# Kernel tuning notes

Hardware: AMD Instinct MI355X
Metric: run time of the kernel (lower is better)

The kernel has to match this reference:

```python
import jax, jax.numpy as jnp
import numpy as np

IN_DIM = 300   # GloVe embedding dim
MEM = 150      # TreeLSTM memory dim
K = 4          # children per internal node (complete K-ary tree)
D = 9          # number of levels (leaves = level 0, root = level D-1)
SIZES = [K ** (D - 1 - d) for d in range(D)]  # nodes per level, leaves first
N = sum(SIZES)  # 87381 total nodes


def setup_inputs() -> dict:
    key = jax.random.key(0)
    ks = jax.random.split(key, 18)
    s_in = 1.0 / np.sqrt(IN_DIM)
    s_m = 1.0 / np.sqrt(MEM)
    inp = {"embs": jax.random.normal(ks[0], (N, IN_DIM), jnp.float32)}
    i = 1
    for nm in ["ix", "fx", "ux", "ox"]:  # input->mem linears
        inp["W_" + nm] = jax.random.uniform(ks[i], (IN_DIM, MEM), jnp.float32, -s_in, s_in); i += 1
        inp["b_" + nm] = jax.random.uniform(ks[i], (MEM,), jnp.float32, -s_in, s_in); i += 1
    for nm in ["ih", "fh", "uh", "oh"]:  # mem->mem linears
        inp["W_" + nm] = jax.random.uniform(ks[i], (MEM, MEM), jnp.float32, -s_m, s_m); i += 1
        inp["b_" + nm] = jax.random.uniform(ks[i], (MEM,), jnp.float32, -s_m, s_m); i += 1
    return inp


def reference(embs, W_ix, b_ix, W_fx, b_fx, W_ux, b_ux, W_ox, b_ox,
              W_ih, b_ih, W_fh, b_fh, W_uh, b_uh, W_oh, b_oh):
    """Level-batched Child-Sum TreeLSTM over a complete K-ary forest.
    Nodes are stored leaves-first; children of parent p at level d are
    nodes p*K .. p*K+K-1 of level d-1. Returns h for all N nodes (root last)."""
    off = 0
    h_prev = c_prev = None
    h_all = []
    for d in range(D):
        n = SIZES[d]
        x = embs[off:off + n]                       # (n, IN_DIM)
        if d == 0:
            # leaves: zero child state -> child_h_sum = 0, f*child_c = 0
            h_sum = jnp.zeros((n, MEM), embs.dtype)
            fc = jnp.zeros((n, MEM), embs.dtype)
        else:
            ch = h_prev.reshape(n, K, MEM)          # child h, (n, K, MEM)
            cc = c_prev.reshape(n, K, MEM)          # child c
            h_sum = ch.sum(axis=1)                  # child-sum of h
            # per-child forget gate: fh(child_h) + fx(x)
            f = jax.nn.sigmoid(jnp.einsum('nkm,mp->nkp', ch, W_fh) + b_fh
                               + (x @ W_fx + b_fx)[:, None, :])
            fc = (f * cc).sum(axis=1)
        i_g = jax.nn.sigmoid(x @ W_ix + b_ix + h_sum @ W_ih + b_ih)
        o_g = jax.nn.sigmoid(x @ W_ox + b_ox + h_sum @ W_oh + b_oh)
        u = jnp.tanh(x @ W_ux + b_ux + h_sum @ W_uh + b_uh)
        c = i_g * u + fc
        h = o_g * jnp.tanh(c)
        h_all.append(h)
        h_prev, c_prev = h, c
        off += n
    return jnp.concatenate(h_all, axis=0)           # (N, MEM)
```

## Files before the change

kernel.cpp:

```cpp
#include <hip/hip_runtime.h>

#define MEM    150
#define GW     640
#define KX     300
#define KXP    320
#define KH     160
#define NLEAF  65536
#define NTOT   87381
#define DEPTH  9

static const int SIZES[DEPTH] = {65536,16384,4096,1024,256,64,16,4,1};
static const int OFF[DEPTH]   = {0,65536,81920,86016,87040,87296,87360,87376,87380};

typedef __attribute__((ext_vector_type(8))) short short8;
typedef __attribute__((ext_vector_type(4))) float f32x4;

__device__ __forceinline__ float sigf(float x) { return 1.0f / (1.0f + __expf(-x)); }
__device__ __forceinline__ float tanhf_fast(float x) {
    float e = __expf(2.0f * x);
    return 1.0f - 2.0f / (e + 1.0f);
}
__device__ __forceinline__ unsigned short f2bf(float f) {
    union { float f; unsigned u; } v; v.f = f;
    unsigned r = v.u + 0x7FFF + ((v.u >> 16) & 1);
    return (unsigned short)(r >> 16);
}
__device__ __forceinline__ float bf2f(unsigned short u) {
    union { unsigned u; float f; } v; v.u = ((unsigned)u) << 16; return v.f;
}

typedef const __attribute__((address_space(1))) unsigned int* as1_u32p;
typedef __attribute__((address_space(3))) unsigned int* as3_u32p;
__device__ __forceinline__ void gl_lds16(const unsigned short* g, unsigned short* l) {
    __builtin_amdgcn_global_load_lds((as1_u32p)g, (as3_u32p)l, 16, 0, 0);
}

__global__ void pack_weights(const float* __restrict__ Wix, const float* __restrict__ Wfx,
                             const float* __restrict__ Wux, const float* __restrict__ Wox,
                             const float* __restrict__ bix, const float* __restrict__ bfx,
                             const float* __restrict__ bux, const float* __restrict__ box,
                             const float* __restrict__ Wih, const float* __restrict__ Wfh,
                             const float* __restrict__ Wuh, const float* __restrict__ Woh,
                             const float* __restrict__ bfh,
                             unsigned short* __restrict__ W4xT, unsigned short* __restrict__ W4hT,
                             float* __restrict__ b4x, float* __restrict__ b4hf)
{
    int stride = gridDim.x * blockDim.x;
    int tid = blockIdx.x * blockDim.x + threadIdx.x;
    for (int idx = tid; idx < GW * KXP; idx += stride) {
        int c = idx / KXP, k = idx - c * KXP;
        int j = c >> 2, g = c & 3;
        const float* W = (g == 0) ? Wix : (g == 1) ? Wfx : (g == 2) ? Wux : Wox;
        W4xT[idx] = (j < MEM && k < KX) ? f2bf(W[k * MEM + j]) : (unsigned short)0;
    }
    for (int idx = tid; idx < GW * KH; idx += stride) {
        int c = idx / KH, k = idx - c * KH;
        int j = c >> 2, g = c & 3;
        const float* W = (g == 0) ? Wih : (g == 1) ? Wfh : (g == 2) ? Wuh : Woh;
        W4hT[idx] = (j < MEM && k < MEM) ? f2bf(W[k * MEM + j]) : (unsigned short)0;
    }
    for (int idx = tid; idx < GW; idx += stride) {
        int j = idx >> 2, g = idx & 3;
        const float* b = (g == 0) ? bix : (g == 1) ? bfx : (g == 2) ? bux : box;
        b4x[idx]  = (j < MEM) ? b[j] : 0.0f;
        b4hf[idx] = (g == 1 && j < MEM) ? bfh[j] : 0.0f;
    }
}

__global__ void conv_embs(const float* __restrict__ embs, unsigned short* __restrict__ Abf)
{
    int idx = blockIdx.x * 256 + threadIdx.x;
    if (idx >= NTOT * (KXP / 8)) return;
    int n = idx / (KXP / 8), c = idx - n * (KXP / 8);
    int c0 = c * 8;
    unsigned short v[8];
    if (c0 + 8 <= KX) {
        const float4* p = (const float4*)(embs + (size_t)n * KX + c0);
        float4 f0 = p[0], f1 = p[1];
        v[0]=f2bf(f0.x); v[1]=f2bf(f0.y); v[2]=f2bf(f0.z); v[3]=f2bf(f0.w);
        v[4]=f2bf(f1.x); v[5]=f2bf(f1.y); v[6]=f2bf(f1.z); v[7]=f2bf(f1.w);
    } else {
        const float* row = embs + (size_t)n * KX;
        #pragma unroll
        for (int j = 0; j < 8; ++j) {
            int col = c0 + j;
            v[j] = (col < KX) ? f2bf(row[col]) : (unsigned short)0;
        }
    }
    *(short8*)&Abf[(size_t)n * KXP + c0] = *(short8*)v;
}

__global__ __launch_bounds__(256) void gemm_xproj(
    const unsigned short* __restrict__ A,
    const unsigned short* __restrict__ BT,
    const float* __restrict__ bias,
    unsigned short* __restrict__ PG,
    const float* __restrict__ bih, const float* __restrict__ buh,
    const float* __restrict__ boh,
    float* __restrict__ outLeaf, float* __restrict__ CLeaf,
    unsigned short* __restrict__ HbfLeaf)
{
    __shared__ __align__(16) unsigned short lds[16384];
    unsigned short* As = lds;
    unsigned short* Bs = lds + 8192;

    const int nwg = gridDim.x;
    const int orig = blockIdx.x;
    const int qq = nwg >> 3, rr = nwg & 7;
    const int xcd = orig & 7, lin = orig >> 3;
    const int dd = (xcd < rr ? xcd * (qq + 1) : rr * (qq + 1) + (xcd - rr) * qq) + lin;
    const int mtile = dd / 5, ntile = dd - mtile * 5;

    const int t = threadIdx.x;
    const int m0 = mtile * 128, n0 = ntile * 128;
    const int l = t & 63, w = t >> 6;
    const int l15 = l & 15, q = l >> 4;
    const int wm = (w & 1) * 64, wn = (w >> 1) * 64;

    const int srow = t >> 2;
    const int scol = ((t & 3) ^ (srow & 3)) * 8;
    int gr0 = m0 + srow;      if (gr0 >= NTOT) gr0 = NTOT - 1;
    int gr1 = m0 + 64 + srow; if (gr1 >= NTOT) gr1 = NTOT - 1;
    const unsigned short* a0 = A + (size_t)gr0 * KXP + scol;
    const unsigned short* a1 = A + (size_t)gr1 * KXP + scol;
    const unsigned short* b0 = BT + (size_t)(n0 + srow) * KXP + scol;
    const unsigned short* b1 = BT + (size_t)(n0 + 64 + srow) * KXP + scol;

    f32x4 acc[4][4];
    #pragma unroll
    for (int i = 0; i < 4; ++i)
        #pragma unroll
        for (int j = 0; j < 4; ++j)
            acc[i][j] = (f32x4){0.f, 0.f, 0.f, 0.f};

    gl_lds16(a0, As + t * 8);
    gl_lds16(a1, As + 2048 + t * 8);
    gl_lds16(b0, Bs + t * 8);
    gl_lds16(b1, Bs + 2048 + t * 8);
    __syncthreads();

    int cur = 0;
    const int kiters = KXP >> 5;
    for (int kt = 0; kt < kiters; ++kt) {
        if (kt + 1 < kiters) {
            const int ko = (kt + 1) << 5;
            const int nb = cur ^ 1;
            gl_lds16(a0 + ko, As + nb * 4096 + t * 8);
            gl_lds16(a1 + ko, As + nb * 4096 + 2048 + t * 8);
            gl_lds16(b0 + ko, Bs + nb * 4096 + t * 8);
            gl_lds16(b1 + ko, Bs + nb * 4096 + 2048 + t * 8);
        }
        short8 a[4], b[4];
        const int csw = (q ^ (l15 & 3)) * 8;
        #pragma unroll
        for (int i = 0; i < 4; ++i)
            a[i] = *(const short8*)&As[cur * 4096 + (wm + i * 16 + l15) * 32 + csw];
        #pragma unroll
        for (int j = 0; j < 4; ++j)
            b[j] = *(const short8*)&Bs[cur * 4096 + (wn + j * 16 + l15) * 32 + csw];
        #pragma unroll
        for (int i = 0; i < 4; ++i)
            #pragma unroll
            for (int j = 0; j < 4; ++j)
                acc[i][j] = __builtin_amdgcn_mfma_f32_16x16x32_bf16(a[i], b[j], acc[i][j], 0, 0, 0);
        __syncthreads();
        cur ^= 1;
    }

    float bj[4];
    #pragma unroll
    for (int j = 0; j < 4; ++j) bj[j] = bias[n0 + wn + j * 16 + l15];
    #pragma unroll
    for (int i = 0; i < 4; ++i)
        #pragma unroll
        for (int j = 0; j < 4; ++j)
            #pragma unroll
            for (int r = 0; r < 4; ++r)
                lds[(wm + i * 16 + q * 4 + r) * 128 + wn + j * 16 + l15] =
                    f2bf(acc[i][j][r] + bj[j]);
    __syncthreads();

    if (m0 < NLEAF) {
        #pragma unroll
        for (int s = 0; s < 16; ++s) {
            int idx = (s << 8) + t;
            int row = idx >> 5, jl = idx & 31;
            int grow = m0 + row;
            int j = ntile * 32 + jl;
            const unsigned short* g4 = &lds[row * 128 + jl * 4];
            if (j < MEM) {
                float gi = bf2f(g4[0]) + bih[j];
                float gu = bf2f(g4[2]) + buh[j];
                float go = bf2f(g4[3]) + boh[j];
                float iv = sigf(gi), uv = tanhf_fast(gu), ov = sigf(go);
                float c = iv * uv;
                float h = ov * tanhf_fast(c);
                outLeaf[(size_t)grow * MEM + j] = h;
                CLeaf[(size_t)grow * MEM + j] = c;
                HbfLeaf[(size_t)grow * KH + j] = f2bf(h);
            } else if (j < KH) {
                HbfLeaf[(size_t)grow * KH + j] = 0;
            }
        }
    } else {
        int row = t >> 1, half = t & 1;
        int grow = m0 + row;
        if (grow < NTOT) {
            const unsigned short* src = &lds[row * 128 + half * 64];
            unsigned short* dst = PG + (size_t)grow * GW + n0 + half * 64;
            #pragma unroll
            for (int c8 = 0; c8 < 8; ++c8)
                *(short8*)(dst + c8 * 8) = *(const short8*)(src + c8 * 8);
        }
    }
}

__global__ __launch_bounds__(256) void gemm_level(
    const unsigned short* __restrict__ Hprev, int nprev, int npar,
    const unsigned short* __restrict__ BT, const float* __restrict__ bias,
    const unsigned short* __restrict__ P,
    const float* __restrict__ Cprev,
    const float* __restrict__ bih, const float* __restrict__ buh,
    const float* __restrict__ boh,
    float* __restrict__ outRow, float* __restrict__ Crow,
    unsigned short* __restrict__ HbfRow)
{
    __shared__ __align__(16) unsigned short lds[16384];
    unsigned short* As = lds;
    unsigned short* Bs = lds + 8192;

    const int nwg = gridDim.x;
    const int orig = blockIdx.x;
    const int qq = nwg >> 3, rr = nwg & 7;
    const int xcd = orig & 7, lin = orig >> 3;
    const int dd = (xcd < rr ? xcd * (qq + 1) : rr * (qq + 1) + (xcd - rr) * qq) + lin;
    const int mtile = dd / 5, ntile = dd - mtile * 5;

    const int t = threadIdx.x;
    const int m0 = mtile * 128, n0 = ntile * 128;
    const int l = t & 63, w = t >> 6;
    const int l15 = l & 15, q = l >> 4;
    const int wm = (w & 1) * 64, wn = (w >> 1) * 64;

    const int srow = t >> 2;
    const int scol = ((t & 3) ^ (srow & 3)) * 8;
    int gr0 = m0 + srow;      if (gr0 >= nprev) gr0 = nprev - 1;
    int gr1 = m0 + 64 + srow; if (gr1 >= nprev) gr1 = nprev - 1;
    const unsigned short* a0 = Hprev + (size_t)gr0 * KH + scol;
    const unsigned short* a1 = Hprev + (size_t)gr1 * KH + scol;
    const unsigned short* b0 = BT + (size_t)(n0 + srow) * KH + scol;
    const unsigned short* b1 = BT + (size_t)(n0 + 64 + srow) * KH + scol;

    f32x4 acc[4][4];
    #pragma unroll
    for (int i = 0; i < 4; ++i)
        #pragma unroll
        for (int j = 0; j < 4; ++j)
            acc[i][j] = (f32x4){0.f, 0.f, 0.f, 0.f};

    gl_lds16(a0, As + t * 8);
    gl_lds16(a1, As + 2048 + t * 8);
    gl_lds16(b0, Bs + t * 8);
    gl_lds16(b1, Bs + 2048 + t * 8);
    __syncthreads();

    int cur = 0;
    const int kiters = KH >> 5;
    for (int kt = 0; kt < kiters; ++kt) {
        if (kt + 1 < kiters) {
            const int ko = (kt + 1) << 5;
            const int nb = cur ^ 1;
            gl_lds16(a0 + ko, As + nb * 4096 + t * 8);
            gl_lds16(a1 + ko, As + nb * 4096 + 2048 + t * 8);
            gl_lds16(b0 + ko, Bs + nb * 4096 + t * 8);
            gl_lds16(b1 + ko, Bs + nb * 4096 + 2048 + t * 8);
        }
        short8 a[4], b[4];
        const int csw = (q ^ (l15 & 3)) * 8;
        #pragma unroll
        for (int i = 0; i < 4; ++i)
            a[i] = *(const short8*)&As[cur * 4096 + (wm + i * 16 + l15) * 32 + csw];
        #pragma unroll
        for (int j = 0; j < 4; ++j)
            b[j] = *(const short8*)&Bs[cur * 4096 + (wn + j * 16 + l15) * 32 + csw];
        #pragma unroll
        for (int i = 0; i < 4; ++i)
            #pragma unroll
            for (int j = 0; j < 4; ++j)
                acc[i][j] = __builtin_amdgcn_mfma_f32_16x16x32_bf16(a[i], b[j], acc[i][j], 0, 0, 0);
        __syncthreads();
        cur ^= 1;
    }

    float bj[4];
    #pragma unroll
    for (int j = 0; j < 4; ++j) bj[j] = bias[n0 + wn + j * 16 + l15];
    #pragma unroll
    for (int i = 0; i < 4; ++i)
        #pragma unroll
        for (int j = 0; j < 4; ++j)
            #pragma unroll
            for (int r = 0; r < 4; ++r)
                lds[(wm + i * 16 + q * 4 + r) * 128 + wn + j * 16 + l15] =
                    f2bf(acc[i][j][r] + bj[j]);
    __syncthreads();

    const int pp0 = m0 >> 2;
    #pragma unroll
    for (int s = 0; s < 4; ++s) {
        int idx = (s << 8) + t;
        int pl = idx >> 5, jl = idx & 31;
        int par = pp0 + pl;
        if (par >= npar) continue;
        int j = ntile * 32 + jl;
        if (j < MEM) {
            const unsigned short* xr = P + (size_t)par * GW + 4 * j;
            float ip = bf2f(xr[0]) + bih[j];
            float fx = bf2f(xr[1]);
            float up = bf2f(xr[2]) + buh[j];
            float op = bf2f(xr[3]) + boh[j];
            float fc = 0.0f;
            #pragma unroll
            for (int k = 0; k < 4; ++k) {
                const unsigned short* g4 = &lds[(pl * 4 + k) * 128 + jl * 4];
                ip += bf2f(g4[0]);
                up += bf2f(g4[2]);
                op += bf2f(g4[3]);
                float f = sigf(fx + bf2f(g4[1]));
                fc += f * Cprev[(size_t)(4 * par + k) * MEM + j];
            }
            float iv = sigf(ip), uv = tanhf_fast(up), ov = sigf(op);
            float c = iv * uv + fc;
            float h = ov * tanhf_fast(c);
            outRow[(size_t)par * MEM + j] = h;
            Crow[(size_t)par * MEM + j] = c;
            HbfRow[(size_t)par * KH + j] = f2bf(h);
        } else if (j < KH) {
            HbfRow[(size_t)par * KH + j] = 0;
        }
    }
}

extern "C" void kernel_launch(void* const* d_in, const int* in_sizes, int n_in,
                              void* d_out, int out_size, void* d_ws, size_t ws_size,
                              hipStream_t stream)
{
    (void)in_sizes; (void)n_in; (void)out_size;
    const float* embs = (const float*)d_in[0];
    const float* Wix = (const float*)d_in[1];  const float* bix = (const float*)d_in[2];
    const float* Wfx = (const float*)d_in[3];  const float* bfx = (const float*)d_in[4];
    const float* Wux = (const float*)d_in[5];  const float* bux = (const float*)d_in[6];
    const float* Wox = (const float*)d_in[7];  const float* box = (const float*)d_in[8];
    const float* Wih = (const float*)d_in[9];  const float* bih = (const float*)d_in[10];
    const float* Wfh = (const float*)d_in[11]; const float* bfh = (const float*)d_in[12];
    const float* Wuh = (const float*)d_in[13]; const float* buh = (const float*)d_in[14];
    const float* Woh = (const float*)d_in[15]; const float* boh = (const float*)d_in[16];
    float* out = (float*)d_out;

    char* p = (char*)d_ws;
    auto alloc = [&](size_t bytes) -> char* {
        char* r = p;
        p += (bytes + 255) & ~(size_t)255;
        return r;
    };
    unsigned short* PG   = (unsigned short*)alloc((size_t)NTOT * GW * 2);
    float*          C    = (float*)alloc((size_t)NTOT * MEM * 4);
    unsigned short* Hbf  = (unsigned short*)alloc((size_t)NTOT * KH * 2);
    unsigned short* W4xT = (unsigned short*)alloc((size_t)GW * KXP * 2);
    unsigned short* W4hT = (unsigned short*)alloc((size_t)GW * KH * 2);
    float*          b4x  = (float*)alloc(GW * 4);
    float*          b4hf = (float*)alloc(GW * 4);
    if ((size_t)(p - (char*)d_ws) > ws_size) return;

    unsigned short* Abf = PG;

    pack_weights<<<128, 256, 0, stream>>>(Wix, Wfx, Wux, Wox, bix, bfx, bux, box,
                                          Wih, Wfh, Wuh, Woh, bfh,
                                          W4xT, W4hT, b4x, b4hf);

    conv_embs<<<(NTOT * (KXP / 8) + 255) / 256, 256, 0, stream>>>(embs, Abf);

    {
        int mt = (NTOT + 127) / 128;
        gemm_xproj<<<mt * 5, 256, 0, stream>>>(
            Abf, W4xT, b4x, PG, bih, buh, boh, out, C, Hbf);
    }

    for (int d = 1; d < DEPTH; ++d) {
        int nprev = SIZES[d - 1];
        int n = SIZES[d];
        int mt = (nprev + 127) / 128;
        gemm_level<<<mt * 5, 256, 0, stream>>>(
            Hbf + (size_t)OFF[d - 1] * KH, nprev, n,
            W4hT, b4hf,
            PG + (size_t)OFF[d] * GW,
            C + (size_t)OFF[d - 1] * MEM,
            bih, buh, boh,
            out + (size_t)OFF[d] * MEM, C + (size_t)OFF[d] * MEM,
            Hbf + (size_t)OFF[d] * KH);
    }
}
```

Before: 371.8 us.

## Merge weight packing and embedding conversion; use 512-thread GEMM blocks with 8 waves

Combines the weight-pack and embedding bf16 conversion kernels into one launch by splitting blocks by index. Both GEMM kernels move from 256 to 512 threads per block. Each of the 8 waves now computes a 64x32 sub-tile instead of 64x64, and each thread issues one A and one B LDS load per k-step instead of two. The aim is to cut per-wave register and accumulator pressure, add more waves to hide latency, and save one launch. The cost is lower MFMA reuse per wave and more waves contending at each block barrier.

Result: faster. 349.9 us (-5.9%).

```diff
diff --git a/kernel.cpp b/kernel.cpp
--- a/kernel.cpp
+++ b/kernel.cpp
@@ -35,62 +35,63 @@
     __builtin_amdgcn_global_load_lds((as1_u32p)g, (as3_u32p)l, 16, 0, 0);
 }
 
-__global__ void pack_weights(const float* __restrict__ Wix, const float* __restrict__ Wfx,
-                             const float* __restrict__ Wux, const float* __restrict__ Wox,
-                             const float* __restrict__ bix, const float* __restrict__ bfx,
-                             const float* __restrict__ bux, const float* __restrict__ box,
-                             const float* __restrict__ Wih, const float* __restrict__ Wfh,
-                             const float* __restrict__ Wuh, const float* __restrict__ Woh,
-                             const float* __restrict__ bfh,
-                             unsigned short* __restrict__ W4xT, unsigned short* __restrict__ W4hT,
-                             float* __restrict__ b4x, float* __restrict__ b4hf)
+__global__ void prep(const float* __restrict__ Wix, const float* __restrict__ Wfx,
+                     const float* __restrict__ Wux, const float* __restrict__ Wox,
+                     const float* __restrict__ bix, const float* __restrict__ bfx,
+                     const float* __restrict__ bux, const float* __restrict__ box,
+                     const float* __restrict__ Wih, const float* __restrict__ Wfh,
+                     const float* __restrict__ Wuh, const float* __restrict__ Woh,
+                     const float* __restrict__ bfh,
+                     const float* __restrict__ embs,
+                     unsigned short* __restrict__ W4xT, unsigned short* __restrict__ W4hT,
+                     float* __restrict__ b4x, float* __restrict__ b4hf,
+                     unsigned short* __restrict__ Abf)
 {
-    int stride = gridDim.x * blockDim.x;
-    int tid = blockIdx.x * blockDim.x + threadIdx.x;
-    for (int idx = tid; idx < GW * KXP; idx += stride) {
-        int c = idx / KXP, k = idx - c * KXP;
-        int j = c >> 2, g = c & 3;
-        const float* W = (g == 0) ? Wix : (g == 1) ? Wfx : (g == 2) ? Wux : Wox;
-        W4xT[idx] = (j < MEM && k < KX) ? f2bf(W[k * MEM + j]) : (unsigned short)0;
-    }
-    for (int idx = tid; idx < GW * KH; idx += stride) {
-        int c = idx / KH, k = idx - c * KH;
-        int j = c >> 2, g = c & 3;
-        const float* W = (g == 0) ? Wih : (g == 1) ? Wfh : (g == 2) ? Wuh : Woh;
-        W4hT[idx] = (j < MEM && k < MEM) ? f2bf(W[k * MEM + j]) : (unsigned short)0;
-    }
-    for (int idx = tid; idx < GW; idx += stride) {
-        int j = idx >> 2, g = idx & 3;
-        const float* b = (g == 0) ? bix : (g == 1) ? bfx : (g == 2) ? bux : box;
-        b4x[idx]  = (j < MEM) ? b[j] : 0.0f;
-        b4hf[idx] = (g == 1 && j < MEM) ? bfh[j] : 0.0f;
-    }
-}
-
-__global__ void conv_embs(const float* __restrict__ embs, unsigned short* __restrict__ Abf)
-{
-    int idx = blockIdx.x * 256 + threadIdx.x;
-    if (idx >= NTOT * (KXP / 8)) return;
-    int n = idx / (KXP / 8), c = idx - n * (KXP / 8);
-    int c0 = c * 8;
-    unsigned short v[8];
-    if (c0 + 8 <= KX) {
-        const float4* p = (const float4*)(embs + (size_t)n * KX + c0);
-        float4 f0 = p[0], f1 = p[1];
-        v[0]=f2bf(f0.x); v[1]=f2bf(f0.y); v[2]=f2bf(f0.z); v[3]=f2bf(f0.w);
-        v[4]=f2bf(f1.x); v[5]=f2bf(f1.y); v[6]=f2bf(f1.z); v[7]=f2bf(f1.w);
+    if (blockIdx.x < 256) {
+        int tid = blockIdx.x * 256 + threadIdx.x;
+        const int stride = 256 * 256;
+        for (int idx = tid; idx < GW * KXP; idx += stride) {
+            int c = idx / KXP, k = idx - c * KXP;
+            int j = c >> 2, g = c & 3;
+            const float* W = (g == 0) ? Wix : (g == 1) ? Wfx : (g == 2) ? Wux : Wox;
+            W4xT[idx] = (j < MEM && k < KX) ? f2bf(W[k * MEM + j]) : (unsigned short)0;
+        }
+        for (int idx = tid; idx < GW * KH; idx += stride) {
+            int c = idx / KH, k = idx - c * KH;
+            int j = c >> 2, g = c & 3;
+            const float* W = (g == 0) ? Wih : (g == 1) ? Wfh : (g == 2) ? Wuh : Woh;
+            W4hT[idx] = (j < MEM && k < MEM) ? f2bf(W[k * MEM + j]) : (unsigned short)0;
+        }
+        for (int idx = tid; idx < GW; idx += stride) {
+            int j = idx >> 2, g = idx & 3;
+            const float* b = (g == 0) ? bix : (g == 1) ? bfx : (g == 2) ? bux : box;
+            b4x[idx]  = (j < MEM) ? b[j] : 0.0f;
+            b4hf[idx] = (g == 1 && j < MEM) ? bfh[j] : 0.0f;
+        }
     } else {
-        const float* row = embs + (size_t)n * KX;
-        #pragma unroll
-        for (int j = 0; j < 8; ++j) {
-            int col = c0 + j;
-            v[j] = (col < KX) ? f2bf(row[col]) : (unsigned short)0;
-        }
-    }
-    *(short8*)&Abf[(size_t)n * KXP + c0] = *(short8*)v;
-}
-
-__global__ __launch_bounds__(256) void gemm_xproj(
+        int idx = (blockIdx.x - 256) * 256 + threadIdx.x;
+        if (idx >= NTOT * (KXP / 8)) return;
+        int n = idx / (KXP / 8), c = idx - n * (KXP / 8);
+        int c0 = c * 8;
+        unsigned short v[8];
+        if (c0 + 8 <= KX) {
+            const float4* p = (const float4*)(embs + (size_t)n * KX + c0);
+            float4 f0 = p[0], f1 = p[1];
+            v[0]=f2bf(f0.x); v[1]=f2bf(f0.y); v[2]=f2bf(f0.z); v[3]=f2bf(f0.w);
+            v[4]=f2bf(f1.x); v[5]=f2bf(f1.y); v[6]=f2bf(f1.z); v[7]=f2bf(f1.w);
+        } else {
+            const float* row = embs + (size_t)n * KX;
+            #pragma unroll
+            for (int j = 0; j < 8; ++j) {
+                int col = c0 + j;
+                v[j] = (col < KX) ? f2bf(row[col]) : (unsigned short)0;
+            }
+        }
+        *(short8*)&Abf[(size_t)n * KXP + c0] = *(short8*)v;
+    }
+}
+
+__global__ __launch_bounds__(512) void gemm_xproj(
     const unsigned short* __restrict__ A,
     const unsigned short* __restrict__ BT,
     const float* __restrict__ bias,
@@ -115,28 +116,23 @@
     const int m0 = mtile * 128, n0 = ntile * 128;
     const int l = t & 63, w = t >> 6;
     const int l15 = l & 15, q = l >> 4;
-    const int wm = (w & 1) * 64, wn = (w >> 1) * 64;
+    const int wm = (w & 1) * 64, wn = (w >> 1) * 32;
 
     const int srow = t >> 2;
     const int scol = ((t & 3) ^ (srow & 3)) * 8;
-    int gr0 = m0 + srow;      if (gr0 >= NTOT) gr0 = NTOT - 1;
-    int gr1 = m0 + 64 + srow; if (gr1 >= NTOT) gr1 = NTOT - 1;
+    int gr0 = m0 + srow; if (gr0 >= NTOT) gr0 = NTOT - 1;
     const unsigned short* a0 = A + (size_t)gr0 * KXP + scol;
-    const unsigned short* a1 = A + (size_t)gr1 * KXP + scol;
     const unsigned short* b0 = BT + (size_t)(n0 + srow) * KXP + scol;
-    const unsigned short* b1 = BT + (size_t)(n0 + 64 + srow) * KXP + scol;
-
-    f32x4 acc[4][4];
+
+    f32x4 acc[4][2];
     #pragma unroll
     for (int i = 0; i < 4; ++i)
         #pragma unroll
-        for (int j = 0; j < 4; ++j)
+        for (int j = 0; j < 2; ++j)
             acc[i][j] = (f32x4){0.f, 0.f, 0.f, 0.f};
 
     gl_lds16(a0, As + t * 8);
-    gl_lds16(a1, As + 2048 + t * 8);
     gl_lds16(b0, Bs + t * 8);
-    gl_lds16(b1, Bs + 2048 + t * 8);
     __syncthreads();
 
     int cur = 0;
@@ -146,34 +142,32 @@
             const int ko = (kt + 1) << 5;
             const int nb = cur ^ 1;
             gl_lds16(a0 + ko, As + nb * 4096 + t * 8);
-            gl_lds16(a1 + ko, As + nb * 4096 + 2048 + t * 8);
             gl_lds16(b0 + ko, Bs + nb * 4096 + t * 8);
-            gl_lds16(b1 + ko, Bs + nb * 4096 + 2048 + t * 8);
-        }
-        short8 a[4], b[4];
+        }
+        short8 a[4], b[2];
         const int csw = (q ^ (l15 & 3)) * 8;
         #pragma unroll
         for (int i = 0; i < 4; ++i)
             a[i] = *(const short8*)&As[cur * 4096 + (wm + i * 16 + l15) * 32 + csw];
         #pragma unroll
-        for (int j = 0; j < 4; ++j)
+        for (int j = 0; j < 2; ++j)
             b[j] = *(const short8*)&Bs[cur * 4096 + (wn + j * 16 + l15) * 32 + csw];
         #pragma unroll
         for (int i = 0; i < 4; ++i)
             #pragma unroll
-            for (int j = 0; j < 4; ++j)
+            for (int j = 0; j < 2; ++j)
                 acc[i][j] = __builtin_amdgcn_mfma_f32_16x16x32_bf16(a[i], b[j], acc[i][j], 0, 0, 0);
         __syncthreads();
         cur ^= 1;
     }
 
-    float bj[4];
-    #pragma unroll
-    for (int j = 0; j < 4; ++j) bj[j] = bias[n0 + wn + j * 16 + l15];
+    float bj[2];
+    #pragma unroll
+    for (int j = 0; j < 2; ++j) bj[j] = bias[n0 + wn + j * 16 + l15];
     #pragma unroll
     for (int i = 0; i < 4; ++i)
         #pragma unroll
-        for (int j = 0; j < 4; ++j)
+        for (int j = 0; j < 2; ++j)
             #pragma unroll
             for (int r = 0; r < 4; ++r)
                 lds[(wm + i * 16 + q * 4 + r) * 128 + wn + j * 16 + l15] =
@@ -182,8 +176,8 @@
 
     if (m0 < NLEAF) {
         #pragma unroll
-        for (int s = 0; s < 16; ++s) {
-            int idx = (s << 8) + t;
+        for (int s = 0; s < 8; ++s) {
+            int idx = (s << 9) + t;
             int row = idx >> 5, jl = idx & 31;
             int grow = m0 + row;
             int j = ntile * 32 + jl;
@@ -203,19 +197,19 @@
             }
         }
     } else {
-        int row = t >> 1, half = t & 1;
+        int row = t >> 2, qd = t & 3;
         int grow = m0 + row;
         if (grow < NTOT) {
-            const unsigned short* src = &lds[row * 128 + half * 64];
-            unsigned short* dst = PG + (size_t)grow * GW + n0 + half * 64;
-            #pragma unroll
-            for (int c8 = 0; c8 < 8; ++c8)
+            const unsigned short* src = &lds[row * 128 + qd * 32];
+            unsigned short* dst = PG + (size_t)grow * GW + n0 + qd * 32;
+            #pragma unroll
+            for (int c8 = 0; c8 < 4; ++c8)
                 *(short8*)(dst + c8 * 8) = *(const short8*)(src + c8 * 8);
         }
     }
 }
 
-__global__ __launch_bounds__(256) void gemm_level(
+__global__ __launch_bounds__(512) void gemm_level(
     const unsigned short* __restrict__ Hprev, int nprev, int npar,
     const unsigned short* __restrict__ BT, const float* __restrict__ bias,
     const unsigned short* __restrict__ P,
@@ -240,28 +234,23 @@
     const int m0 = mtile * 128, n0 = ntile * 128;
     const int l = t & 63, w = t >> 6;
     const int l15 = l & 15, q = l >> 4;
-    const int wm = (w & 1) * 64, wn = (w >> 1) * 64;
+    const int wm = (w & 1) * 64, wn = (w >> 1) * 32;
 
     const int srow = t >> 2;
     const int scol = ((t & 3) ^ (srow & 3)) * 8;
-    int gr0 = m0 + srow;      if (gr0 >= nprev) gr0 = nprev - 1;
-    int gr1 = m0 + 64 + srow; if (gr1 >= nprev) gr1 = nprev - 1;
+    int gr0 = m0 + srow; if (gr0 >= nprev) gr0 = nprev - 1;
     const unsigned short* a0 = Hprev + (size_t)gr0 * KH + scol;
-    const unsigned short* a1 = Hprev + (size_t)gr1 * KH + scol;
     const unsigned short* b0 = BT + (size_t)(n0 + srow) * KH + scol;
-    const unsigned short* b1 = BT + (size_t)(n0 + 64 + srow) * KH + scol;
-
-    f32x4 acc[4][4];
+
+    f32x4 acc[4][2];
     #pragma unroll
     for (int i = 0; i < 4; ++i)
         #pragma unroll
-        for (int j = 0; j < 4; ++j)
+        for (int j = 0; j < 2; ++j)
             acc[i][j] = (f32x4){0.f, 0.f, 0.f, 0.f};
 
     gl_lds16(a0, As + t * 8);
-    gl_lds16(a1, As + 2048 + t * 8);
     gl_lds16(b0, Bs + t * 8);
-    gl_lds16(b1, Bs + 2048 + t * 8);
     __syncthreads();
 
     int cur = 0;
@@ -271,34 +260,32 @@
             const int ko = (kt + 1) << 5;
             const int nb = cur ^ 1;
             gl_lds16(a0 + ko, As + nb * 4096 + t * 8);
-            gl_lds16(a1 + ko, As + nb * 4096 + 2048 + t * 8);
             gl_lds16(b0 + ko, Bs + nb * 4096 + t * 8);
-            gl_lds16(b1 + ko, Bs + nb * 4096 + 2048 + t * 8);
-        }
-        short8 a[4], b[4];
+        }
+        short8 a[4], b[2];
         const int csw = (q ^ (l15 & 3)) * 8;
         #pragma unroll
         for (int i = 0; i < 4; ++i)
             a[i] = *(const short8*)&As[cur * 4096 + (wm + i * 16 + l15) * 32 + csw];
         #pragma unroll
-        for (int j = 0; j < 4; ++j)
+        for (int j = 0; j < 2; ++j)
             b[j] = *(const short8*)&Bs[cur * 4096 + (wn + j * 16 + l15) * 32 + csw];
         #pragma unroll
         for (int i = 0; i < 4; ++i)
             #pragma unroll
-            for (int j = 0; j < 4; ++j)
+            for (int j = 0; j < 2; ++j)
                 acc[i][j] = __builtin_amdgcn_mfma_f32_16x16x32_bf16(a[i], b[j], acc[i][j], 0, 0, 0);
         __syncthreads();
         cur ^= 1;
     }
 
-    float bj[4];
-    #pragma unroll
-    for (int j = 0; j < 4; ++j) bj[j] = bias[n0 + wn + j * 16 + l15];
+    float bj[2];
+    #pragma unroll
+    for (int j = 0; j < 2; ++j) bj[j] = bias[n0 + wn + j * 16 + l15];
     #pragma unroll
     for (int i = 0; i < 4; ++i)
         #pragma unroll
-        for (int j = 0; j < 4; ++j)
+        for (int j = 0; j < 2; ++j)
             #pragma unroll
             for (int r = 0; r < 4; ++r)
                 lds[(wm + i * 16 + q * 4 + r) * 128 + wn + j * 16 + l15] =
@@ -307,8 +294,8 @@
 
     const int pp0 = m0 >> 2;
     #pragma unroll
-    for (int s = 0; s < 4; ++s) {
-        int idx = (s << 8) + t;
+    for (int s = 0; s < 2; ++s) {
+        int idx = (s << 9) + t;
         int pl = idx >> 5, jl = idx & 31;
         int par = pp0 + pl;
         if (par >= npar) continue;
@@ -374,15 +361,17 @@
 
     unsigned short* Abf = PG;
 
-    pack_weights<<<128, 256, 0, stream>>>(Wix, Wfx, Wux, Wox, bix, bfx, bux, box,
-                                          Wih, Wfh, Wuh, Woh, bfh,
-                                          W4xT, W4hT, b4x, b4hf);
-
-    conv_embs<<<(NTOT * (KXP / 8) + 255) / 256, 256, 0, stream>>>(embs, Abf);
+    {
+        int convBlocks = (NTOT * (KXP / 8) + 255) / 256;
+        prep<<<256 + convBlocks, 256, 0, stream>>>(
+            Wix, Wfx, Wux, Wox, bix, bfx, bux, box,
+            Wih, Wfh, Wuh, Woh, bfh, embs,
+            W4xT, W4hT, b4x, b4hf, Abf);
+    }
 
     {
         int mt = (NTOT + 127) / 128;
-        gemm_xproj<<<mt * 5, 256, 0, stream>>>(
+        gemm_xproj<<<mt * 5, 512, 0, stream>>>(
             Abf, W4xT, b4x, PG, bih, buh, boh, out, C, Hbf);
     }
 
@@ -390,7 +379,7 @@
         int nprev = SIZES[d - 1];
         int n = SIZES[d];
         int mt = (nprev + 127) / 128;
-        gemm_level<<<mt * 5, 256, 0, stream>>>(
+        gemm_level<<<mt * 5, 512, 0, stream>>>(
             Hbf + (size_t)OFF[d - 1] * KH, nprev, n,
             W4hT, b4hf,
             PG + (size_t)OFF[d] * GW,
```
